# Kernel tuning notes

Measured on AMD Instinct MI355X. Metric: run time of the kernel, lower is better.

The kernel has to match this reference:

```python
import jax, jax.numpy as jnp
import numpy as np

C_IN = 144
PC = 288           # proj_channels = 2 * in_channels
HEADS = 12
DG = 12            # deformable groups
CLIP = 2
KH = KW = 3
A = KH * KW        # samples per clip per group (attention window 3x3)
PAD = 1
MAXMAG = 10.0
B, T, H, W = 1, 1, 64, 64


def _conv2d(x, w, b, pad):
    y = jax.lax.conv_general_dilated(x, w, (1, 1), [(pad, pad), (pad, pad)],
                                     dimension_numbers=('NCHW', 'OIHW', 'NCHW'))
    return y + b[None, :, None, None]


def _lrelu(x):
    return jnp.where(x >= 0, x, 0.1 * x)


def _linear_c(x, w, b):
    # per-pixel linear on channel dim; x: (..., Cin, h, w), w: (Cin, Cout)
    return jnp.einsum('...ihw,io->...ohw', x, w) + b[:, None, None]


def _bilinear_gather(feat, py, px):
    # feat: (b, clip, g, cg, h, w); py/px: (b, clip, g, A, h, w) absolute pixel coords
    # zero padding outside image (deformable-conv sampling semantics)
    b, cl, g, cg, h, w = feat.shape
    ff = feat.reshape(b, cl, g, cg, h * w)
    y0 = jnp.floor(py)
    x0 = jnp.floor(px)
    wy1 = py - y0
    wx1 = px - x0

    def corner(yc, xc, wt):
        valid = ((yc >= 0) & (yc < h) & (xc >= 0) & (xc < w)).astype(feat.dtype)
        yi = jnp.clip(yc, 0, h - 1).astype(jnp.int32)
        xi = jnp.clip(xc, 0, w - 1).astype(jnp.int32)
        idx = (yi * w + xi).reshape(b, cl, g, 1, -1)
        gat = jnp.take_along_axis(ff, idx, axis=-1).reshape(b, cl, g, cg, *py.shape[3:])
        return gat * (wt * valid)[:, :, :, None]

    out = corner(y0, x0, (1 - wy1) * (1 - wx1))
    out = out + corner(y0, x0 + 1, (1 - wy1) * wx1)
    out = out + corner(y0 + 1, x0, wy1 * (1 - wx1))
    out = out + corner(y0 + 1, x0 + 1, wy1 * wx1)
    return out  # (b, clip, g, cg, A, h, w)


def setup_inputs() -> dict:
    key = jax.random.key(0)
    ks = jax.random.split(key, 32)
    rn = lambda i, shp, s=1.0: jax.random.normal(ks[i], shp, dtype=jnp.float32) * s
    cin_off = C_IN * (1 + CLIP) + CLIP * 2   # 436
    c_off = CLIP * DG * A * 2                # 432
    d = {
        'q': rn(0, (B, T, C_IN, H, W)),
        'k': rn(1, (B, CLIP, C_IN, H, W)),
        'v': rn(2, (B, CLIP, C_IN, H, W)),
        'vpw0': rn(3, (B, T, C_IN, H, W)),
        'vpw1': rn(4, (B, T, C_IN, H, W)),
        'flow0': rn(5, (B, T, 2, H, W), 3.0),
        'flow1': rn(6, (B, T, 2, H, W), 3.0),
        'wo1': rn(7, (64, cin_off, 1, 1), 1.0 / np.sqrt(cin_off)),
        'bo1': rn(8, (64,), 0.01),
        'wo2': rn(9, (64, 64, 3, 3), 1.0 / np.sqrt(64 * 9)),
        'bo2': rn(10, (64,), 0.01),
        'wo3': rn(11, (64, 64, 3, 3), 1.0 / np.sqrt(64 * 9)),
        'bo3': rn(12, (64,), 0.01),
        'wo4': rn(13, (64, 64, 3, 3), 1.0 / np.sqrt(64 * 9)),
        'bo4': rn(14, (64,), 0.01),
        'wo5': rn(15, (64, 64, 3, 3), 1.0 / np.sqrt(64 * 9)),
        'bo5': rn(16, (64,), 0.01),
        'wo6': rn(17, (c_off, 64, 1, 1), 0.02),
        'bo6': rn(18, (c_off,), 0.01),
        'wq': rn(19, (C_IN, PC), 1.0 / np.sqrt(C_IN)),
        'bq': rn(20, (PC,), 0.01),
        'wk': rn(21, (C_IN, PC), 1.0 / np.sqrt(C_IN)),
        'bk': rn(22, (PC,), 0.01),
        'wv': rn(23, (C_IN, PC), 1.0 / np.sqrt(C_IN)),
        'bv': rn(24, (PC,), 0.01),
        'wp': rn(25, (PC, C_IN), 1.0 / np.sqrt(PC)),
        'bp': rn(26, (C_IN,), 0.01),
        'wm1': rn(27, (C_IN, 2 * C_IN), 1.0 / np.sqrt(C_IN)),
        'bm1': rn(28, (2 * C_IN,), 0.01),
        'wm2': rn(29, (2 * C_IN, C_IN), 1.0 / np.sqrt(2 * C_IN)),
        'bm2': rn(30, (C_IN,), 0.01),
    }
    return d


def reference(q, k, v, vpw0, vpw1, flow0, flow1,
              wo1, bo1, wo2, bo2, wo3, bo3, wo4, bo4, wo5, bo5, wo6, bo6,
              wq, bq, wk, bk, wv, bv, wp, bp, wm1, bm1, wm2, bm2):
    b, t, c, h, w = q.shape  # t == 1 here so q batch b*t matches kv batch b
    bt = b * t
    # --- offset predictor: Conv3d stack with time-kernel 1 == 2D convs ---
    x = jnp.concatenate([q, vpw0, vpw1, flow0, flow1], axis=2).reshape(bt, -1, h, w)
    x = _lrelu(_conv2d(x, wo1, bo1, 0))
    x = _lrelu(_conv2d(x, wo2, bo2, 1))
    x = _lrelu(_conv2d(x, wo3, bo3, 1))
    x = _lrelu(_conv2d(x, wo4, bo4, 1))
    x = _lrelu(_conv2d(x, wo5, bo5, 1))
    off = MAXMAG * jnp.tanh(_conv2d(x, wo6, bo6, 0))  # (bt, CLIP*DG*A*2, h, w)
    # add optical flow (channel-flipped to (y, x)) to every sample offset
    fyx = flow0.reshape(bt, 2, h, w)[:, ::-1]
    off = off + jnp.tile(fyx, (1, off.shape[1] // 2, 1, 1))
    off = off.reshape(bt, CLIP, DG, A, 2, h, w)
    ar = jnp.arange(A)
    by = (ar // KW - PAD).astype(q.dtype)  # kernel base offsets (stride=1, dil=1)
    bx = (ar % KW - PAD).astype(q.dtype)
    py = off[:, :, :, :, 0] + by[None, None, None, :, None, None] \
         + jnp.arange(h, dtype=q.dtype)[:, None]
    px = off[:, :, :, :, 1] + bx[None, None, None, :, None, None] \
         + jnp.arange(w, dtype=q.dtype)
    # --- q/k/v projections ---
    hd = PC // HEADS
    qp = _linear_c(q, wq, bq).reshape(bt, HEADS, hd, h, w)
    kp = _linear_c(k, wk, bk).reshape(b, CLIP, DG, PC // DG, h, w)
    vp = _linear_c(v, wv, bv).reshape(b, CLIP, DG, PC // DG, h, w)
    # --- deformable bilinear gather (per deformable group) ---
    ksamp = _bilinear_gather(kp, py, px).reshape(bt, CLIP, HEADS, hd, A, h, w)
    vsamp = _bilinear_gather(vp, py, px).reshape(bt, CLIP, HEADS, hd, A, h, w)
    # --- attention over CLIP*A sampled locations, per pixel per head ---
    scores = jnp.einsum('bmdyx,bcmdayx->bmcayx', qp, ksamp) * (hd ** -0.5)
    attn = jax.nn.softmax(scores.reshape(bt, HEADS, CLIP * A, h, w), axis=2)
    vflat = vsamp.transpose(0, 2, 1, 4, 3, 5, 6).reshape(bt, HEADS, CLIP * A, hd, h, w)
    out = jnp.einsum('bmsyx,bmsdyx->bmdyx', attn, vflat).reshape(b, t, PC, h, w)
    # --- output projection + MLP residual ---
    o = _linear_c(out, wp, bp)
    m = _linear_c(jax.nn.gelu(_linear_c(o, wm1, bm1), approximate=False), wm2, bm2)
    return o + m
```

## Files before the change

### kernel.cpp

```cpp
#include <hip/hip_runtime.h>
#include <hip/hip_bf16.h>
#include <math.h>

typedef __hip_bfloat16 bf16;
typedef __attribute__((ext_vector_type(8))) short bf16x8v;
typedef __attribute__((ext_vector_type(4))) float f32x4v;

#define NPIX 4096

__device__ __forceinline__ float b2f(bf16 v) { return __bfloat162float(v); }
__device__ __forceinline__ unsigned short f2bu(float f) {
    bf16 h = __float2bfloat16(f);
    return *(unsigned short*)&h;
}
__device__ __forceinline__ int detect_bf16(const unsigned short* __restrict__ qraw) {
    int lane = threadIdx.x & 63;
    unsigned short u = qraw[lane * 2];
    int e = (u >> 7) & 0xFF;
    unsigned long long ball = __ballot(e >= 100 && e <= 135);
    return __popcll(ball) > 32;
}
__device__ __forceinline__ float rdval(const void* s, int idx, int isbf) {
    return isbf ? b2f(((const bf16*)s)[idx]) : ((const float*)s)[idx];
}

#define OF_WO6 175680
#define OF_BO6 203328
#define OF_BO1 27904
#define OF_BO2 64832
#define OF_BO3 101760
#define OF_BO4 138688
#define OF_BO5 175616
#define OF_BQ  245232
#define OF_BK  286992
#define OF_BV  328752
#define OF_BP  370512
#define OF_BM1 412128
#define OF_BM2 453888
#define OF_FL0 454032

struct CArgs { const void* src[14]; int dstoff[14]; int n[14]; };
struct PPJob { const void* src; int dstS; int Mp, Kp, kr, mr, sstride, kind; };
struct PPArgs { PPJob j[11]; };

__global__ void misc_kernel(CArgs a, PPArgs pa, const void* __restrict__ q,
                            const void* __restrict__ k, const void* __restrict__ v,
                            const void* __restrict__ vp0, const void* __restrict__ vp1,
                            const void* __restrict__ fl0, const void* __restrict__ fl1,
                            float* __restrict__ cw, short* __restrict__ XS,
                            short* __restrict__ X1, short* __restrict__ wsS)
{
    const int isbf = detect_bf16((const unsigned short*)q);
    const int y = blockIdx.y;
    if (y < 14) {
        const int n = a.n[y];
        float* d = cw + a.dstoff[y];
        if (isbf) {
            const bf16* s = (const bf16*)a.src[y];
            for (int i = blockIdx.x * 256 + threadIdx.x; i < n; i += 256 * 16) d[i] = b2f(s[i]);
        } else {
            const float* s = (const float*)a.src[y];
            for (int i = blockIdx.x * 256 + threadIdx.x; i < n; i += 256 * 16) d[i] = s[i];
        }
    } else if (y < 24) {
        const int job = y - 14;
        const int z = job >> 1, half = job & 1;
        const int p = blockIdx.x * 256 + threadIdx.x;
        const void* srcs[5] = { q, k, k, v, v };
        const int clips[5] = { 0, 0, 1, 0, 1 };
        const size_t co = (size_t)clips[z] * 144 * NPIX;
        short* row = XS + (size_t)z * 655360 + (size_t)p * 160;
        for (int c0 = half * 72; c0 < half * 72 + 72; c0 += 8) {
            unsigned short h[8];
            if (isbf) {
                const bf16* s = (const bf16*)srcs[z] + co;
#pragma unroll
                for (int i = 0; i < 8; ++i) h[i] = f2bu(b2f(s[(size_t)(c0 + i) * NPIX + p]));
            } else {
                const float* s = (const float*)srcs[z] + co;
#pragma unroll
                for (int i = 0; i < 8; ++i) h[i] = f2bu(s[(size_t)(c0 + i) * NPIX + p]);
            }
            uint4 u;
            u.x = (unsigned)h[0] | ((unsigned)h[1] << 16);
            u.y = (unsigned)h[2] | ((unsigned)h[3] << 16);
            u.z = (unsigned)h[4] | ((unsigned)h[5] << 16);
            u.w = (unsigned)h[6] | ((unsigned)h[7] << 16);
            *(uint4*)(row + c0) = u;
        }
        if (half == 1) {
            uint4 zz; zz.x = zz.y = zz.z = zz.w = 0u;
            *(uint4*)(row + 144) = zz;
            *(uint4*)(row + 152) = zz;
        }
    } else if (y < 28) {
        const int sec = y - 24;
        const int p = blockIdx.x * 256 + threadIdx.x;
        short* row = X1 + (size_t)p * 448;
        if (sec < 3) {
            const void* srcs[3] = { q, vp0, vp1 };
            const int cbase = sec * 144;
            for (int c0 = 0; c0 < 144; c0 += 8) {
                unsigned short h[8];
                if (isbf) {
                    const bf16* s = (const bf16*)srcs[sec];
#pragma unroll
                    for (int i = 0; i < 8; ++i) h[i] = f2bu(b2f(s[(size_t)(c0 + i) * NPIX + p]));
                } else {
                    const float* s = (const float*)srcs[sec];
#pragma unroll
                    for (int i = 0; i < 8; ++i) h[i] = f2bu(s[(size_t)(c0 + i) * NPIX + p]);
                }
                uint4 u;
                u.x = (unsigned)h[0] | ((unsigned)h[1] << 16);
                u.y = (unsigned)h[2] | ((unsigned)h[3] << 16);
                u.z = (unsigned)h[4] | ((unsigned)h[5] << 16);
                u.w = (unsigned)h[6] | ((unsigned)h[7] << 16);
                *(uint4*)(row + cbase + c0) = u;
            }
        } else {
            unsigned short h[4];
            if (isbf) {
                const bf16* f0 = (const bf16*)fl0;
                const bf16* f1 = (const bf16*)fl1;
                h[0] = f2bu(b2f(f0[p]));
                h[1] = f2bu(b2f(f0[NPIX + p]));
                h[2] = f2bu(b2f(f1[p]));
                h[3] = f2bu(b2f(f1[NPIX + p]));
            } else {
                const float* f0 = (const float*)fl0;
                const float* f1 = (const float*)fl1;
                h[0] = f2bu(f0[p]);
                h[1] = f2bu(f0[NPIX + p]);
                h[2] = f2bu(f1[p]);
                h[3] = f2bu(f1[NPIX + p]);
            }
            uint4 u;
            u.x = (unsigned)h[0] | ((unsigned)h[1] << 16);
            u.y = (unsigned)h[2] | ((unsigned)h[3] << 16);
            u.z = 0u; u.w = 0u;
            *(uint4*)(row + 432) = u;
            uint4 zz; zz.x = zz.y = zz.z = zz.w = 0u;
            *(uint4*)(row + 440) = zz;
        }
    } else {
        PPJob J = pa.j[y - 28];
        const int tot = J.Mp * J.Kp;
        for (int e = blockIdx.x * 256 + threadIdx.x; e < tot; e += 256 * 16) {
            int m = e / J.Kp, kk = e - m * J.Kp;
            float vv = 0.f;
            if (J.kind == 0) { if (kk < J.kr) vv = rdval(J.src, m * J.sstride + kk, isbf); }
            else if (J.kind == 1) { if (kk < J.kr && m < J.mr) vv = rdval(J.src, kk * J.sstride + m, isbf); }
            else { int c = kk & 63, tap = kk >> 6; if (kk < J.kr) vv = rdval(J.src, m * J.sstride + c * 9 + tap, isbf); }
            wsS[J.dstS + e] = (short)f2bu(vv);
        }
    }
}

struct GemmDesc {
    const short* A; const short* B; const float* bias;
    void* dst; void* dst2; const unsigned short* qraw;
    int Mp, Mreal, mode, gofs, ostride, obase, nwaves;
};
struct GemmDesc5 { GemmDesc d[5]; };

template <int TM, int TN, int BM, int KP>
__global__ __launch_bounds__(256) void gemm_kernel(GemmDesc5 gd)
{
    const GemmDesc d = gd.d[blockIdx.z];
    const int wid = blockIdx.x * 4 + (threadIdx.x >> 6);
    if (wid >= d.nwaves) return;
    const int lane = threadIdx.x & 63;
    const int tiles_m = d.Mp / (16 * TM);
    const int m0 = (wid % tiles_m) * (16 * TM);
    const int p0 = (wid / tiles_m) * (16 * TN);
    const int ar = lane & 15;
    const int kq = (lane >> 4) * 8;

    f32x4v acc[TM][TN];
#pragma unroll
    for (int i = 0; i < TM; ++i)
#pragma unroll
        for (int j = 0; j < TN; ++j) acc[i][j] = (f32x4v){0.f, 0.f, 0.f, 0.f};

#pragma unroll
    for (int k0 = 0; k0 < KP; k0 += 32) {
        bf16x8v a[TM], b[TN];
#pragma unroll
        for (int i = 0; i < TM; ++i)
            a[i] = *(const bf16x8v*)(d.A + (size_t)(m0 + i * 16 + ar) * KP + k0 + kq);
        if (BM == 0) {
#pragma unroll
            for (int j = 0; j < TN; ++j)
                b[j] = *(const bf16x8v*)(d.B + (size_t)(p0 + j * 16 + ar) * KP + k0 + kq);
        } else {
            const int tap = k0 >> 6;
            const int cc = (k0 & 63) + kq;
            const int dy = tap / 3 - 1, dx = tap % 3 - 1;
#pragma unroll
            for (int j = 0; j < TN; ++j) {
                const int pix = p0 + j * 16 + ar;
                const int yy = (pix >> 6) + dy, xx = (pix & 63) + dx;
                const bool ok = ((unsigned)yy < 64u) & ((unsigned)xx < 64u);
                const int np = min(max(yy, 0), 63) * 64 + min(max(xx, 0), 63);
                bf16x8v bv = *(const bf16x8v*)(d.B + (size_t)np * 64 + cc);
                if (!ok) bv = (bf16x8v)(short)0;
                b[j] = bv;
            }
        }
#pragma unroll
        for (int i = 0; i < TM; ++i)
#pragma unroll
            for (int j = 0; j < TN; ++j)
                acc[i][j] = __builtin_amdgcn_mfma_f32_16x16x32_bf16(a[i], b[j], acc[i][j], 0, 0, 0);
    }

    const int isbf = (d.mode == 5) ? detect_bf16(d.qraw) : 0;
#pragma unroll
    for (int i = 0; i < TM; ++i) {
#pragma unroll
        for (int j = 0; j < TN; ++j) {
            const int pcol = p0 + j * 16 + (lane & 15);
            const int mb = m0 + i * 16 + (lane >> 4) * 4;
            float vv[4];
#pragma unroll
            for (int r = 0; r < 4; ++r) {
                const int m = mb + r;
                vv[r] = acc[i][j][r];
                if (m < d.Mreal) vv[r] += d.bias[m];
            }
            if (d.mode == 0) {
#pragma unroll
                for (int r = 0; r < 4; ++r) vv[r] = (vv[r] >= 0.f) ? vv[r] : 0.1f * vv[r];
                uint2 u;
                u.x = (unsigned)f2bu(vv[0]) | ((unsigned)f2bu(vv[1]) << 16);
                u.y = (unsigned)f2bu(vv[2]) | ((unsigned)f2bu(vv[3]) << 16);
                *(uint2*)((unsigned short*)d.dst + (size_t)pcol * d.Mp + mb) = u;
            } else if (d.mode == 1) {
                const int g = mb / 24 + d.gofs;
                uint2 u;
                u.x = (unsigned)f2bu(vv[0]) | ((unsigned)f2bu(vv[1]) << 16);
                u.y = (unsigned)f2bu(vv[2]) | ((unsigned)f2bu(vv[3]) << 16);
                *(uint2*)((unsigned short*)d.dst +
                          ((size_t)g * NPIX + pcol) * d.ostride + (mb % 24) + d.obase) = u;
            } else if (d.mode == 3) {
                uint2 u;
                u.x = (unsigned)f2bu(vv[0]) | ((unsigned)f2bu(vv[1]) << 16);
                u.y = (unsigned)f2bu(vv[2]) | ((unsigned)f2bu(vv[3]) << 16);
                *(uint2*)((unsigned short*)d.dst + (size_t)pcol * 160 + mb) = u;
                if (mb < 144)
                    *(float4*)((float*)d.dst2 + (size_t)pcol * 144 + mb) =
                        make_float4(vv[0], vv[1], vv[2], vv[3]);
            } else if (d.mode == 4) {
#pragma unroll
                for (int r = 0; r < 4; ++r)
                    vv[r] = 0.5f * vv[r] * (1.f + erff(vv[r] * 0.70710678118654752f));
                uint2 u;
                u.x = (unsigned)f2bu(vv[0]) | ((unsigned)f2bu(vv[1]) << 16);
                u.y = (unsigned)f2bu(vv[2]) | ((unsigned)f2bu(vv[3]) << 16);
                *(uint2*)((unsigned short*)d.dst + (size_t)pcol * d.Mp + mb) = u;
            } else {
#pragma unroll
                for (int r = 0; r < 4; ++r) {
                    const int m = mb + r;
                    if (m < 144) {
                        float v = vv[r] + ((float*)d.dst2)[(size_t)pcol * 144 + m];
                        if (isbf) ((unsigned short*)d.dst)[(size_t)m * NPIX + pcol] = f2bu(v);
                        else      ((float*)d.dst)[(size_t)m * NPIX + pcol] = v;
                    }
                }
            }
        }
    }
}

__global__ __launch_bounds__(256) void conv6_kernel(const short* __restrict__ YF,
                                                    const float* __restrict__ cw,
                                                    float* __restrict__ pyx)
{
    const int p = blockIdx.x * 256 + threadIdx.x;
    const int o0 = blockIdx.y * 16;
    const uint4* yrow = (const uint4*)(YF + (size_t)p * 64);
    const float* wb = cw + OF_WO6 + o0 * 64;

    float acc[16];
#pragma unroll
    for (int j = 0; j < 16; ++j) acc[j] = cw[OF_BO6 + o0 + j];

#pragma unroll
    for (int c = 0; c < 8; ++c) {
        uint4 u = yrow[c];
        float a0 = __uint_as_float(u.x << 16);
        float a1 = __uint_as_float(u.x & 0xFFFF0000u);
        float a2 = __uint_as_float(u.y << 16);
        float a3 = __uint_as_float(u.y & 0xFFFF0000u);
        float a4 = __uint_as_float(u.z << 16);
        float a5 = __uint_as_float(u.z & 0xFFFF0000u);
        float a6 = __uint_as_float(u.w << 16);
        float a7 = __uint_as_float(u.w & 0xFFFF0000u);
#pragma unroll
        for (int j = 0; j < 16; ++j) {
            const float* wr = wb + j * 64 + c * 8;
            acc[j] += a0 * wr[0] + a1 * wr[1] + a2 * wr[2] + a3 * wr[3]
                    + a4 * wr[4] + a5 * wr[5] + a6 * wr[6] + a7 * wr[7];
        }
    }

    const float f_y = cw[OF_FL0 + NPIX + p];
    const float f_x = cw[OF_FL0 + p];
    const float yf = (float)(p >> 6), xf = (float)(p & 63);
#pragma unroll
    for (int j = 0; j < 16; j += 2) {
        const int s = (o0 + j) >> 1;
        const int a_idx = s % 9;
        float vy = 10.f * tanhf(acc[j]);
        float vx = 10.f * tanhf(acc[j + 1]);
        float2 o;
        o.x = vy + f_y + (float)(a_idx / 3 - 1) + yf;
        o.y = vx + f_x + (float)(a_idx % 3 - 1) + xf;
        *(float2*)(pyx + 2 * ((size_t)s * NPIX + p)) = o;
    }
}

__device__ __forceinline__ float dot12(const bf16* __restrict__ row, const float* qv) {
    const uint2* s = (const uint2*)row;
    float d = 0.f;
#pragma unroll
    for (int c = 0; c < 3; ++c) {
        uint2 u = s[c];
        d += qv[c * 4 + 0] * __uint_as_float(u.x << 16);
        d += qv[c * 4 + 1] * __uint_as_float(u.x & 0xFFFF0000u);
        d += qv[c * 4 + 2] * __uint_as_float(u.y << 16);
        d += qv[c * 4 + 3] * __uint_as_float(u.y & 0xFFFF0000u);
    }
    return d;
}
__device__ __forceinline__ void acc12(float* ov, const bf16* __restrict__ row, float f) {
    const uint2* s = (const uint2*)row;
#pragma unroll
    for (int c = 0; c < 3; ++c) {
        uint2 u = s[c];
        ov[c * 4 + 0] += f * __uint_as_float(u.x << 16);
        ov[c * 4 + 1] += f * __uint_as_float(u.x & 0xFFFF0000u);
        ov[c * 4 + 2] += f * __uint_as_float(u.y << 16);
        ov[c * 4 + 3] += f * __uint_as_float(u.y & 0xFFFF0000u);
    }
}

__global__ __launch_bounds__(256) void attn_kernel(
    const bf16* __restrict__ qp, const bf16* __restrict__ kv,
    const float* __restrict__ pyx, unsigned short* __restrict__ att)
{
    const int t = blockIdx.x * 256 + threadIdx.x;
    const int ch = t & 1;
    const int clip = (t >> 1) & 1;
    const int sh = (t >> 2) & 1;
    const int pp = t >> 3;
    const int m = pp >> 12;
    const int p = pp & 4095;

    float qv[12];
    {
        const uint2* s = (const uint2*)(qp + (size_t)(m * 4096 + p) * 24 + ch * 12);
#pragma unroll
        for (int c = 0; c < 3; ++c) {
            uint2 u = s[c];
            qv[c * 4 + 0] = __uint_as_float(u.x << 16);
            qv[c * 4 + 1] = __uint_as_float(u.x & 0xFFFF0000u);
            qv[c * 4 + 2] = __uint_as_float(u.y << 16);
            qv[c * 4 + 3] = __uint_as_float(u.y & 0xFFFF0000u);
        }
    }

    const int gidx = clip * 12 + m;
    const bf16* kvb = kv + (size_t)gidx * 4096 * 48 + ch * 12;
    const int sbase = gidx * 9;
    const int a0 = sh ? 5 : 0;
    const int na = sh ? 4 : 5;

    float e[5], fyv[5], fxv[5];
    float mx = -1e30f;
#pragma unroll
    for (int i = 0; i < 5; ++i) {
        e[i] = -1e30f; fyv[i] = 0.f; fxv[i] = 0.f;
        if (i < na) {
            const int a = a0 + i;
            const float2 f2v = *(const float2*)(pyx + 2 * ((size_t)(sbase + a) * NPIX + p));
            const float fy = f2v.x, fx = f2v.y;
            fyv[i] = fy; fxv[i] = fx;
            const float y0 = floorf(fy), x0 = floorf(fx);
            const float wy = fy - y0, wx = fx - x0;
            const int iy = (int)y0, ix = (int)x0;
            const float w00 = (1.f - wy) * (1.f - wx), w01 = (1.f - wy) * wx;
            const float w10 = wy * (1.f - wx), w11 = wy * wx;
            float part = 0.f;
            if ((unsigned)iy < 64u) {
                const bf16* rr = kvb + (size_t)(iy * 64) * 48;
                if ((unsigned)ix < 64u)       part += w00 * dot12(rr + ix * 48, qv);
                if ((unsigned)(ix + 1) < 64u) part += w01 * dot12(rr + (ix + 1) * 48, qv);
            }
            if ((unsigned)(iy + 1) < 64u) {
                const bf16* rr = kvb + (size_t)((iy + 1) * 64) * 48;
                if ((unsigned)ix < 64u)       part += w10 * dot12(rr + ix * 48, qv);
                if ((unsigned)(ix + 1) < 64u) part += w11 * dot12(rr + (ix + 1) * 48, qv);
            }
            float full = part + __shfl_xor(part, 1, 64);
            e[i] = full * 0.20412414523193154f;
            mx = fmaxf(mx, e[i]);
        }
    }
    mx = fmaxf(mx, __shfl_xor(mx, 4, 64));
    mx = fmaxf(mx, __shfl_xor(mx, 2, 64));
    float sum = 0.f;
#pragma unroll
    for (int i = 0; i < 5; ++i) {
        if (i < na) { e[i] = __expf(e[i] - mx); sum += e[i]; }
    }
    sum += __shfl_xor(sum, 4, 64);
    sum += __shfl_xor(sum, 2, 64);
    const float inv = 1.f / sum;

    float ov[12];
#pragma unroll
    for (int j = 0; j < 12; ++j) ov[j] = 0.f;

#pragma unroll
    for (int i = 0; i < 5; ++i) {
        if (i < na) {
            const float wa = e[i] * inv;
            const float fy = fyv[i], fx = fxv[i];
            const float y0 = floorf(fy), x0 = floorf(fx);
            const float wy = fy - y0, wx = fx - x0;
            const int iy = (int)y0, ix = (int)x0;
            if ((unsigned)iy < 64u) {
                const bf16* rr = kvb + (size_t)(iy * 64) * 48 + 24;
                if ((unsigned)ix < 64u)       acc12(ov, rr + ix * 48, wa * (1.f - wy) * (1.f - wx));
                if ((unsigned)(ix + 1) < 64u) acc12(ov, rr + (ix + 1) * 48, wa * (1.f - wy) * wx);
            }
            if ((unsigned)(iy + 1) < 64u) {
                const bf16* rr = kvb + (size_t)((iy + 1) * 64) * 48 + 24;
                if ((unsigned)ix < 64u)       acc12(ov, rr + ix * 48, wa * wy * (1.f - wx));
                if ((unsigned)(ix + 1) < 64u) acc12(ov, rr + (ix + 1) * 48, wa * wy * wx);
            }
        }
    }
#pragma unroll
    for (int j = 0; j < 12; ++j) {
        ov[j] += __shfl_xor(ov[j], 4, 64);
        ov[j] += __shfl_xor(ov[j], 2, 64);
    }
    if (clip == 0 && sh == 0) {
        unsigned short* ab = att + (size_t)p * 288 + m * 24 + ch * 12;
#pragma unroll
        for (int c = 0; c < 3; ++c) {
            uint2 u;
            u.x = (unsigned)f2bu(ov[c * 4 + 0]) | ((unsigned)f2bu(ov[c * 4 + 1]) << 16);
            u.y = (unsigned)f2bu(ov[c * 4 + 2]) | ((unsigned)f2bu(ov[c * 4 + 3]) << 16);
            ((uint2*)ab)[c] = u;
        }
    }
}

__global__ void diag_kernel(float* __restrict__ out, int n, float v)
{
    int i = blockIdx.x * 256 + threadIdx.x;
    if (i < n) out[i] = (i == 0 ? v : 0.f);
}

extern "C" void kernel_launch(void* const* d_in, const int* in_sizes, int n_in,
                              void* d_out, int out_size, void* d_ws, size_t ws_size,
                              hipStream_t stream)
{
    const size_t REQUIRED = 75000000;
    if (ws_size < REQUIRED) {
        float code = 1000.0f + (float)(ws_size >> 20);
        diag_kernel<<<dim3((out_size + 255) / 256), 256, 0, stream>>>((float*)d_out, out_size, code);
        return;
    }

    char* W = (char*)d_ws;
    short* wsS = (short*)W;
    float* cw = (float*)(W + 64);

    short* conv1w = wsS + 1000000;
    short* conv3w[4] = { wsS + 1028672, wsS + 1065536, wsS + 1102400, wsS + 1139264 };
    short* wqb = wsS + 1176128, *wkb = wsS + 1222208, *wvb = wsS + 1268288;
    short* wpS = wsS + 1314368, *wm1S = wsS + 1360448, *wm2S = wsS + 1406528;

    short* XS = (short*)(W + 16777216);
    short* X1 = (short*)(W + 25165824);
    bf16*  QP = (bf16*)(W + 33554432);
    bf16*  KV = (bf16*)(W + 36700160);
    short* Y0 = (short*)(W + 50331648);
    short* Y1 = (short*)(W + 50855936);
    short* YF = (short*)(W + 51380224);
    float* PYX = (float*)(W + 54525952);
    unsigned short* ATT = (unsigned short*)(W + 62914560);
    short* OPM = (short*)(W + 67108864);
    float* O32 = (float*)(W + 68419584);
    short* M1  = (short*)(W + 71303168);

    const unsigned short* qraw = (const unsigned short*)d_in[0];

    CArgs ca;
    const int srcidx[14] = {8,10,12,14,16,17,18,20,22,24,26,28,30,5};
    const int dsto[14]   = {OF_BO1,OF_BO2,OF_BO3,OF_BO4,OF_BO5,OF_WO6,OF_BO6,
                            OF_BQ,OF_BK,OF_BV,OF_BP,OF_BM1,OF_BM2,OF_FL0};
    for (int i = 0; i < 14; ++i) {
        ca.src[i] = d_in[srcidx[i]];
        ca.dstoff[i] = dsto[i];
        ca.n[i] = in_sizes[srcidx[i]];
    }
    PPArgs pp;
    pp.j[0]  = { d_in[7],  1000000, 64, 448, 436, 64,  436, 0 };
    pp.j[1]  = { d_in[9],  1028672, 64, 576, 576, 64,  576, 2 };
    pp.j[2]  = { d_in[11], 1065536, 64, 576, 576, 64,  576, 2 };
    pp.j[3]  = { d_in[13], 1102400, 64, 576, 576, 64,  576, 2 };
    pp.j[4]  = { d_in[15], 1139264, 64, 576, 576, 64,  576, 2 };
    pp.j[5]  = { d_in[19], 1176128, 288, 160, 144, 288, 288, 1 };
    pp.j[6]  = { d_in[21], 1222208, 288, 160, 144, 288, 288, 1 };
    pp.j[7]  = { d_in[23], 1268288, 288, 160, 144, 288, 288, 1 };
    pp.j[8]  = { d_in[25], 1314368, 160, 288, 288, 144, 144, 1 };
    pp.j[9]  = { d_in[27], 1360448, 288, 160, 144, 288, 288, 1 };
    pp.j[10] = { d_in[29], 1406528, 160, 288, 288, 144, 144, 1 };
    misc_kernel<<<dim3(16, 39), 256, 0, stream>>>(ca, pp, d_in[0], d_in[1], d_in[2], d_in[3],
                                                  d_in[4], d_in[5], d_in[6], cw, XS, X1, wsS);

    GemmDesc5 g3;
    const short* Xz[5] = { XS, XS + 655360, XS + 1310720, XS + 1966080, XS + 2621440 };
    const short* Az[5] = { wqb, wkb, wkb, wvb, wvb };
    const float* Bz[5] = { cw + OF_BQ, cw + OF_BK, cw + OF_BK, cw + OF_BV, cw + OF_BV };
    bf16* Dz[5] = { QP, KV, KV, KV, KV };
    const int Gz[5] = { 0, 0, 12, 0, 12 };
    const int Oz[5] = { 24, 48, 48, 48, 48 };
    const int Bo[5] = { 0, 0, 0, 24, 24 };
    for (int z = 0; z < 5; ++z)
        g3.d[z] = { Az[z], Xz[z], Bz[z], Dz[z], nullptr, qraw, 288, 288, 1, Gz[z], Oz[z], Bo[z], 1152 };
    gemm_kernel<2, 2, 0, 160><<<dim3(288, 1, 5), 256, 0, stream>>>(g3);

    GemmDesc5 g1;
    g1.d[0] = { conv1w, X1, cw + OF_BO1, Y0, nullptr, qraw, 64, 64, 0, 0, 0, 0, 1024 };
    gemm_kernel<1, 1, 0, 448><<<dim3(256, 1, 1), 256, 0, stream>>>(g1);

    const float* cb[4] = { cw + OF_BO2, cw + OF_BO3, cw + OF_BO4, cw + OF_BO5 };
    short* cin[4] = { Y0, Y1, Y0, Y1 };
    short* coutp[4] = { Y1, Y0, Y1, YF };
    for (int i = 0; i < 4; ++i) {
        GemmDesc5 gc;
        gc.d[0] = { conv3w[i], cin[i], cb[i], coutp[i], nullptr, qraw, 64, 64, 0, 0, 0, 0, 1024 };
        gemm_kernel<1, 1, 1, 576><<<dim3(256, 1, 1), 256, 0, stream>>>(gc);
    }

    conv6_kernel<<<dim3(16, 27), 256, 0, stream>>>(YF, cw, PYX);

    attn_kernel<<<dim3(1536), 256, 0, stream>>>(QP, KV, PYX, ATT);

    GemmDesc5 gwp;
    gwp.d[0] = { wpS, (const short*)ATT, cw + OF_BP, OPM, O32, qraw, 160, 144, 3, 0, 0, 0, 640 };
    gemm_kernel<2, 2, 0, 288><<<dim3(160, 1, 1), 256, 0, stream>>>(gwp);

    GemmDesc5 gm1;
    gm1.d[0] = { wm1S, OPM, cw + OF_BM1, M1, nullptr, qraw, 288, 288, 4, 0, 0, 0, 1152 };
    gemm_kernel<2, 2, 0, 160><<<dim3(288, 1, 1), 256, 0, stream>>>(gm1);

    GemmDesc5 gm2;
    gm2.d[0] = { wm2S, M1, cw + OF_BM2, d_out, O32, qraw, 160, 144, 5, 0, 0, 0, 640 };
    gemm_kernel<2, 2, 0, 288><<<dim3(160, 1, 1), 256, 0, stream>>>(gm2);
}
```

Before: 285.8 us.

## Split K/V into separate buffers and spread attention samples over 4 threads

The attention kernel now assigns each (pixel, head, clip, channel-half) to four threads instead of two, each handling 2-3 of the 9 samples, doubling the grid and adding one more shuffle level to the reductions. The projection GEMM writes K and V into separate contiguous 24-channel buffers instead of one interleaved 48-wide buffer, so the key and value gathers touch denser rows. The goal is more parallelism and latency hiding in the gather-bound attention stage, at the cost of more threads, duplicated q loads and extra cross-lane shuffles.

```diff
diff --git a/kernel.cpp b/kernel.cpp
--- a/kernel.cpp
+++ b/kernel.cpp
@@ -348,15 +348,16 @@
 }
 
 __global__ __launch_bounds__(256) void attn_kernel(
-    const bf16* __restrict__ qp, const bf16* __restrict__ kv,
-    const float* __restrict__ pyx, unsigned short* __restrict__ att)
+    const bf16* __restrict__ qp, const bf16* __restrict__ kp,
+    const bf16* __restrict__ vp, const float* __restrict__ pyx,
+    unsigned short* __restrict__ att)
 {
     const int t = blockIdx.x * 256 + threadIdx.x;
     const int ch = t & 1;
     const int clip = (t >> 1) & 1;
-    const int sh = (t >> 2) & 1;
-    const int pp = t >> 3;
-    const int m = pp >> 12;
+    const int sq = (t >> 2) & 3;
+    const int pp = t >> 4;
+    const int m = pp / 4096;
     const int p = pp & 4095;
 
     float qv[12];
@@ -373,15 +374,16 @@
     }
 
     const int gidx = clip * 12 + m;
-    const bf16* kvb = kv + (size_t)gidx * 4096 * 48 + ch * 12;
+    const bf16* kb = kp + (size_t)gidx * 4096 * 24 + ch * 12;
+    const bf16* vb = vp + (size_t)gidx * 4096 * 24 + ch * 12;
     const int sbase = gidx * 9;
-    const int a0 = sh ? 5 : 0;
-    const int na = sh ? 4 : 5;
-
-    float e[5], fyv[5], fxv[5];
+    const int a0 = (sq == 0) ? 0 : (sq * 2 + 1);
+    const int na = (sq == 0) ? 3 : 2;
+
+    float e[3], fyv[3], fxv[3];
     float mx = -1e30f;
 #pragma unroll
-    for (int i = 0; i < 5; ++i) {
+    for (int i = 0; i < 3; ++i) {
         e[i] = -1e30f; fyv[i] = 0.f; fxv[i] = 0.f;
         if (i < na) {
             const int a = a0 + i;
@@ -395,27 +397,29 @@
             const float w10 = wy * (1.f - wx), w11 = wy * wx;
             float part = 0.f;
             if ((unsigned)iy < 64u) {
-                const bf16* rr = kvb + (size_t)(iy * 64) * 48;
-                if ((unsigned)ix < 64u)       part += w00 * dot12(rr + ix * 48, qv);
-                if ((unsigned)(ix + 1) < 64u) part += w01 * dot12(rr + (ix + 1) * 48, qv);
+                const bf16* rr = kb + (size_t)(iy * 64) * 24;
+                if ((unsigned)ix < 64u)       part += w00 * dot12(rr + ix * 24, qv);
+                if ((unsigned)(ix + 1) < 64u) part += w01 * dot12(rr + (ix + 1) * 24, qv);
             }
             if ((unsigned)(iy + 1) < 64u) {
-                const bf16* rr = kvb + (size_t)((iy + 1) * 64) * 48;
-                if ((unsigned)ix < 64u)       part += w10 * dot12(rr + ix * 48, qv);
-                if ((unsigned)(ix + 1) < 64u) part += w11 * dot12(rr + (ix + 1) * 48, qv);
+                const bf16* rr = kb + (size_t)((iy + 1) * 64) * 24;
+                if ((unsigned)ix < 64u)       part += w10 * dot12(rr + ix * 24, qv);
+                if ((unsigned)(ix + 1) < 64u) part += w11 * dot12(rr + (ix + 1) * 24, qv);
             }
             float full = part + __shfl_xor(part, 1, 64);
             e[i] = full * 0.20412414523193154f;
             mx = fmaxf(mx, e[i]);
         }
     }
+    mx = fmaxf(mx, __shfl_xor(mx, 8, 64));
     mx = fmaxf(mx, __shfl_xor(mx, 4, 64));
     mx = fmaxf(mx, __shfl_xor(mx, 2, 64));
     float sum = 0.f;
 #pragma unroll
-    for (int i = 0; i < 5; ++i) {
+    for (int i = 0; i < 3; ++i) {
         if (i < na) { e[i] = __expf(e[i] - mx); sum += e[i]; }
     }
+    sum += __shfl_xor(sum, 8, 64);
     sum += __shfl_xor(sum, 4, 64);
     sum += __shfl_xor(sum, 2, 64);
     const float inv = 1.f / sum;
@@ -425,7 +429,7 @@
     for (int j = 0; j < 12; ++j) ov[j] = 0.f;
 
 #pragma unroll
-    for (int i = 0; i < 5; ++i) {
+    for (int i = 0; i < 3; ++i) {
         if (i < na) {
             const float wa = e[i] * inv;
             const float fy = fyv[i], fx = fxv[i];
@@ -433,23 +437,24 @@
             const float wy = fy - y0, wx = fx - x0;
             const int iy = (int)y0, ix = (int)x0;
             if ((unsigned)iy < 64u) {
-                const bf16* rr = kvb + (size_t)(iy * 64) * 48 + 24;
-                if ((unsigned)ix < 64u)       acc12(ov, rr + ix * 48, wa * (1.f - wy) * (1.f - wx));
-                if ((unsigned)(ix + 1) < 64u) acc12(ov, rr + (ix + 1) * 48, wa * (1.f - wy) * wx);
+                const bf16* rr = vb + (size_t)(iy * 64) * 24;
+                if ((unsigned)ix < 64u)       acc12(ov, rr + ix * 24, wa * (1.f - wy) * (1.f - wx));
+                if ((unsigned)(ix + 1) < 64u) acc12(ov, rr + (ix + 1) * 24, wa * (1.f - wy) * wx);
             }
             if ((unsigned)(iy + 1) < 64u) {
-                const bf16* rr = kvb + (size_t)((iy + 1) * 64) * 48 + 24;
-                if ((unsigned)ix < 64u)       acc12(ov, rr + ix * 48, wa * wy * (1.f - wx));
-                if ((unsigned)(ix + 1) < 64u) acc12(ov, rr + (ix + 1) * 48, wa * wy * wx);
+                const bf16* rr = vb + (size_t)((iy + 1) * 64) * 24;
+                if ((unsigned)ix < 64u)       acc12(ov, rr + ix * 24, wa * wy * (1.f - wx));
+                if ((unsigned)(ix + 1) < 64u) acc12(ov, rr + (ix + 1) * 24, wa * wy * wx);
             }
         }
     }
 #pragma unroll
     for (int j = 0; j < 12; ++j) {
+        ov[j] += __shfl_xor(ov[j], 8, 64);
         ov[j] += __shfl_xor(ov[j], 4, 64);
         ov[j] += __shfl_xor(ov[j], 2, 64);
     }
-    if (clip == 0 && sh == 0) {
+    if (clip == 0 && sq == 0) {
         unsigned short* ab = att + (size_t)p * 288 + m * 24 + ch * 12;
 #pragma unroll
         for (int c = 0; c < 3; ++c) {
@@ -490,7 +495,8 @@
     short* XS = (short*)(W + 16777216);
     short* X1 = (short*)(W + 25165824);
     bf16*  QP = (bf16*)(W + 33554432);
-    bf16*  KV = (bf16*)(W + 36700160);
+    bf16*  KP = (bf16*)(W + 36700160);
+    bf16*  VP = (bf16*)(W + 41943040);
     short* Y0 = (short*)(W + 50331648);
     short* Y1 = (short*)(W + 50855936);
     short* YF = (short*)(W + 51380224);
@@ -530,12 +536,10 @@
     const short* Xz[5] = { XS, XS + 655360, XS + 1310720, XS + 1966080, XS + 2621440 };
     const short* Az[5] = { wqb, wkb, wkb, wvb, wvb };
     const float* Bz[5] = { cw + OF_BQ, cw + OF_BK, cw + OF_BK, cw + OF_BV, cw + OF_BV };
-    bf16* Dz[5] = { QP, KV, KV, KV, KV };
+    bf16* Dz[5] = { QP, KP, KP, VP, VP };
     const int Gz[5] = { 0, 0, 12, 0, 12 };
-    const int Oz[5] = { 24, 48, 48, 48, 48 };
-    const int Bo[5] = { 0, 0, 0, 24, 24 };
     for (int z = 0; z < 5; ++z)
-        g3.d[z] = { Az[z], Xz[z], Bz[z], Dz[z], nullptr, qraw, 288, 288, 1, Gz[z], Oz[z], Bo[z], 1152 };
+        g3.d[z] = { Az[z], Xz[z], Bz[z], Dz[z], nullptr, qraw, 288, 288, 1, Gz[z], 24, 0, 1152 };
     gemm_kernel<2, 2, 0, 160><<<dim3(288, 1, 5), 256, 0, stream>>>(g3);
 
     GemmDesc5 g1;
@@ -553,7 +557,7 @@
 
     conv6_kernel<<<dim3(16, 27), 256, 0, stream>>>(YF, cw, PYX);
 
-    attn_kernel<<<dim3(1536), 256, 0, stream>>>(QP, KV, PYX, ATT);
+    attn_kernel<<<dim3(3072), 256, 0, stream>>>(QP, KP, VP, PYX, ATT);
 
     GemmDesc5 gwp;
     gwp.d[0] = { wpS, (const short*)ATT, cw + OF_BP, OPM, O32, qraw, 160, 144, 3, 0, 0, 0, 640 };
```

New measurement: 274.4 us. 1.04x faster.
